# Kernel optimization log

Measured on AMD Instinct MI355X. Metric: run time of the kernel, lower is better.

Reference implementation:

```python
import jax, jax.numpy as jnp
import numpy as np

B, H, S, DK = 2, 16, 2048, 64
NEG = jnp.float32(-10000.0)


def setup_inputs() -> dict:
    key = jax.random.key(0)
    kq, kk, kv, km = jax.random.split(key, 4)
    query = jax.random.normal(kq, (B, H, S, DK), dtype=jnp.float32)
    k_ = jax.random.normal(kk, (B, H, S, DK), dtype=jnp.float32)
    value = jax.random.normal(kv, (B, H, S, DK), dtype=jnp.float32)
    mask = (jax.random.uniform(km, (B, 1, S, S)) > 0.5).astype(jnp.float32)
    return {"query": query, "key": k_, "value": value, "mask": mask, "d_k": DK}


def reference(query, key, value, mask, d_k):
    # scores: [B,H,S,S]
    scale = jnp.float32(1.0 / np.sqrt(d_k))
    scores = jnp.einsum('bhqd,bhkd->bhqk', query, key) * scale * mask
    # non-standard masking: keep only strictly positive masked scores
    scores = jnp.where(scores > 0, scores, NEG)
    attn = jax.nn.softmax(scores, axis=-1)
    return jnp.einsum('bhqk,bhkd->bhqd', attn, value)
```

## Files before the change

### kernel.cpp

```cpp
#include <hip/hip_runtime.h>
#include <hip/hip_bf16.h>
#include <math.h>

#define S_LEN 2048
#define D_KV  64
#define BQ    128
#define BK    64
#define LP    72
#define NW    8

typedef __attribute__((ext_vector_type(8))) short bh8;
typedef __attribute__((ext_vector_type(4))) short sh4;
typedef __attribute__((ext_vector_type(4))) float fx4;

__device__ __forceinline__ short f2bf(float f) {
    unsigned u = __builtin_bit_cast(unsigned, f);
    u += 0x7fffu + ((u >> 16) & 1u);
    return (short)(u >> 16);
}

__global__ __launch_bounds__(512, 4)
void attn_fwd(const float* __restrict__ Qg, const float* __restrict__ Kg,
              const float* __restrict__ Vg, const float* __restrict__ Mg,
              float* __restrict__ Og)
{
    __shared__ __align__(16) short k_lds[BK * LP];
    __shared__ __align__(16) short v_lds[D_KV * LP];
    __shared__ __align__(16) short p_lds[NW * 16 * LP];

    const int tid  = threadIdx.x;
    const int wave = tid >> 6;
    const int lane = tid & 63;
    const int g    = lane >> 4;
    const int c    = lane & 15;

    const int qt = blockIdx.x;
    const int bh = blockIdx.y;
    const int b  = bh >> 4;

    const int qw = qt * BQ + wave * 16;

    const float* Qp = Qg + ((size_t)bh * S_LEN + qw) * D_KV;
    const float* Kp = Kg + (size_t)bh * S_LEN * D_KV;
    const float* Vp = Vg + (size_t)bh * S_LEN * D_KV;
    const float* Mp = Mg + (size_t)b * S_LEN * S_LEN;
    float*       Op = Og + ((size_t)bh * S_LEN + qw) * D_KV;

    bh8 qf[2];
#pragma unroll
    for (int kc = 0; kc < 2; ++kc) {
        const float* src = Qp + c * D_KV + kc * 32 + g * 8;
        float4 a0 = *(const float4*)(src);
        float4 a1 = *(const float4*)(src + 4);
        bh8 f;
        f[0] = f2bf(a0.x * 0.125f); f[1] = f2bf(a0.y * 0.125f);
        f[2] = f2bf(a0.z * 0.125f); f[3] = f2bf(a0.w * 0.125f);
        f[4] = f2bf(a1.x * 0.125f); f[5] = f2bf(a1.y * 0.125f);
        f[6] = f2bf(a1.z * 0.125f); f[7] = f2bf(a1.w * 0.125f);
        qf[kc] = f;
    }

    fx4 o[4];
    float l_r[4];
#pragma unroll
    for (int u = 0; u < 4; ++u) { fx4 z = {0.f, 0.f, 0.f, 0.f}; o[u] = z; }
#pragma unroll
    for (int r = 0; r < 4; ++r) l_r[r] = 0.f;

    for (int kt = 0; kt < S_LEN; kt += BK) {
#pragma unroll
        for (int i = 0; i < 2; ++i) {
            int idx = tid + 512 * i;
            int kr  = idx >> 4;
            int db  = (idx & 15) * 4;
            float4 kv = *(const float4*)(Kp + (size_t)(kt + kr) * D_KV + db);
            sh4 s4;
            s4[0] = f2bf(kv.x); s4[1] = f2bf(kv.y);
            s4[2] = f2bf(kv.z); s4[3] = f2bf(kv.w);
            *(sh4*)&k_lds[kr * LP + db] = s4;
        }
        {
            int kr = lane;
#pragma unroll
            for (int i = 0; i < 2; ++i) {
                int db = wave * 8 + i * 4;
                float4 vv = *(const float4*)(Vp + (size_t)(kt + kr) * D_KV + db);
                v_lds[(db + 0) * LP + kr] = f2bf(vv.x);
                v_lds[(db + 1) * LP + kr] = f2bf(vv.y);
                v_lds[(db + 2) * LP + kr] = f2bf(vv.z);
                v_lds[(db + 3) * LP + kr] = f2bf(vv.w);
            }
        }
        __syncthreads();

        fx4 sacc[4];
#pragma unroll
        for (int t = 0; t < 4; ++t) { fx4 z = {0.f, 0.f, 0.f, 0.f}; sacc[t] = z; }
#pragma unroll
        for (int kc = 0; kc < 2; ++kc) {
#pragma unroll
            for (int t = 0; t < 4; ++t) {
                bh8 kf = *(const bh8*)&k_lds[(t * 16 + c) * LP + kc * 32 + g * 8];
                sacc[t] = __builtin_amdgcn_mfma_f32_16x16x32_bf16(qf[kc], kf, sacc[t], 0, 0, 0);
            }
        }

        const float* mbase = Mp + (size_t)(qw + g * 4) * S_LEN + kt + c;
        float mv[4][4];
#pragma unroll
        for (int t = 0; t < 4; ++t)
#pragma unroll
            for (int r = 0; r < 4; ++r)
                mv[t][r] = mbase[(size_t)r * S_LEN + t * 16];

        short* pw = &p_lds[wave * 16 * LP];
#pragma unroll
        for (int t = 0; t < 4; ++t)
#pragma unroll
            for (int r = 0; r < 4; ++r) {
                float tm = sacc[t][r] * mv[t][r];
                float p  = (tm > 0.f) ? __expf(tm) : 0.f;
                l_r[r] += p;
                pw[(g * 4 + r) * LP + t * 16 + c] = f2bf(p);
            }

#pragma unroll
        for (int kc = 0; kc < 2; ++kc) {
            bh8 pa = *(const bh8*)&pw[c * LP + kc * 32 + g * 8];
#pragma unroll
            for (int u = 0; u < 4; ++u) {
                bh8 vb = *(const bh8*)&v_lds[(u * 16 + c) * LP + kc * 32 + g * 8];
                o[u] = __builtin_amdgcn_mfma_f32_16x16x32_bf16(pa, vb, o[u], 0, 0, 0);
            }
        }
        __syncthreads();
    }

#pragma unroll
    for (int r = 0; r < 4; ++r) {
#pragma unroll
        for (int off = 8; off >= 1; off >>= 1)
            l_r[r] += __shfl_xor(l_r[r], off, 16);
    }

#pragma unroll
    for (int r = 0; r < 4; ++r) {
        float inv = 1.0f / l_r[r];
#pragma unroll
        for (int u = 0; u < 4; ++u)
            Op[(size_t)(g * 4 + r) * D_KV + u * 16 + c] = o[u][r] * inv;
    }
}

extern "C" void kernel_launch(void* const* d_in, const int* in_sizes, int n_in,
                              void* d_out, int out_size, void* d_ws, size_t ws_size,
                              hipStream_t stream) {
    const float* Q = (const float*)d_in[0];
    const float* K = (const float*)d_in[1];
    const float* V = (const float*)d_in[2];
    const float* M = (const float*)d_in[3];
    float*       O = (float*)d_out;
    dim3 grid(S_LEN / BQ, 32);
    attn_fwd<<<grid, 512, 0, stream>>>(Q, K, V, M, O);
}
```

Measured before the change: 188.6 us.

## Split KV range across wave groups, transpose MFMA, keep P in registers

Halves the query tile to 64 rows and splits the 2048-long key range between two groups of four waves, then merges partial outputs and row sums through shared memory at the end. Swaps the MFMA operand order so the probability tile comes out in the register layout needed as the B operand of the PV product, removing the P round-trip through LDS. It also moves K/V staging to XOR-swizzled LDS without padding, uses packed bf16 conversion instructions, and loads the mask as vector float4 rows. Costs include the extra merge step and more blocks contending for mask bandwidth.

```diff
diff --git a/kernel.cpp b/kernel.cpp
--- a/kernel.cpp
+++ b/kernel.cpp
@@ -1,154 +1,179 @@
 #include <hip/hip_runtime.h>
-#include <hip/hip_bf16.h>
 #include <math.h>
 
 #define S_LEN 2048
 #define D_KV  64
-#define BQ    128
+#define BQ    64
 #define BK    64
-#define LP    72
-#define NW    8
+#define KHALF 1024
 
 typedef __attribute__((ext_vector_type(8))) short bh8;
-typedef __attribute__((ext_vector_type(4))) short sh4;
 typedef __attribute__((ext_vector_type(4))) float fx4;
+typedef __attribute__((ext_vector_type(4))) unsigned int u32x4;
+typedef __attribute__((ext_vector_type(2))) unsigned int u32x2;
 
-__device__ __forceinline__ short f2bf(float f) {
-    unsigned u = __builtin_bit_cast(unsigned, f);
-    u += 0x7fffu + ((u >> 16) & 1u);
-    return (short)(u >> 16);
+__device__ __forceinline__ unsigned cvt2(float a, float b) {
+    unsigned r;
+    asm("v_cvt_pk_bf16_f32 %0, %1, %2" : "=v"(r) : "v"(a), "v"(b));
+    return r;
 }
 
-__global__ __launch_bounds__(512, 4)
+__device__ __forceinline__ int kswz(int row, int dkb) {
+    return ((row << 7) + dkb) ^ ((row & 7) << 4);
+}
+__device__ __forceinline__ int vswz(int d, int colb) {
+    return ((d << 7) + colb) ^ (((d >> 2) & 7) << 4);
+}
+
+__global__ __launch_bounds__(512, 6)
 void attn_fwd(const float* __restrict__ Qg, const float* __restrict__ Kg,
               const float* __restrict__ Vg, const float* __restrict__ Mg,
               float* __restrict__ Og)
 {
-    __shared__ __align__(16) short k_lds[BK * LP];
-    __shared__ __align__(16) short v_lds[D_KV * LP];
-    __shared__ __align__(16) short p_lds[NW * 16 * LP];
+    __shared__ __align__(16) char smem[32768];
 
     const int tid  = threadIdx.x;
     const int wave = tid >> 6;
     const int lane = tid & 63;
     const int g    = lane >> 4;
     const int c    = lane & 15;
+    const int kg   = wave >> 2;
+    const int tidg = tid & 255;
 
     const int qt = blockIdx.x;
     const int bh = blockIdx.y;
     const int b  = bh >> 4;
 
-    const int qw = qt * BQ + wave * 16;
+    const int qbase = qt * BQ + (wave & 3) * 16;
 
-    const float* Qp = Qg + ((size_t)bh * S_LEN + qw) * D_KV;
+    short* kb = (short*)(smem) + kg * 4096;
+    short* vb = (short*)(smem + 16384) + kg * 4096;
+
     const float* Kp = Kg + (size_t)bh * S_LEN * D_KV;
     const float* Vp = Vg + (size_t)bh * S_LEN * D_KV;
-    const float* Mp = Mg + (size_t)b * S_LEN * S_LEN;
-    float*       Op = Og + ((size_t)bh * S_LEN + qw) * D_KV;
+    const float* Qp = Qg + ((size_t)bh * S_LEN + qbase) * D_KV;
+    const float* mrow = Mg + (size_t)b * S_LEN * S_LEN
+                      + (size_t)(qbase + c) * S_LEN + g * 4;
 
     bh8 qf[2];
 #pragma unroll
     for (int kc = 0; kc < 2; ++kc) {
         const float* src = Qp + c * D_KV + kc * 32 + g * 8;
-        float4 a0 = *(const float4*)(src);
-        float4 a1 = *(const float4*)(src + 4);
-        bh8 f;
-        f[0] = f2bf(a0.x * 0.125f); f[1] = f2bf(a0.y * 0.125f);
-        f[2] = f2bf(a0.z * 0.125f); f[3] = f2bf(a0.w * 0.125f);
-        f[4] = f2bf(a1.x * 0.125f); f[5] = f2bf(a1.y * 0.125f);
-        f[6] = f2bf(a1.z * 0.125f); f[7] = f2bf(a1.w * 0.125f);
-        qf[kc] = f;
+        fx4 a0 = *(const fx4*)(src);
+        fx4 a1 = *(const fx4*)(src + 4);
+        u32x4 q4 = { cvt2(a0[0] * 0.125f, a0[1] * 0.125f),
+                     cvt2(a0[2] * 0.125f, a0[3] * 0.125f),
+                     cvt2(a1[0] * 0.125f, a1[1] * 0.125f),
+                     cvt2(a1[2] * 0.125f, a1[3] * 0.125f) };
+        qf[kc] = __builtin_bit_cast(bh8, q4);
     }
 
     fx4 o[4];
-    float l_r[4];
 #pragma unroll
     for (int u = 0; u < 4; ++u) { fx4 z = {0.f, 0.f, 0.f, 0.f}; o[u] = z; }
+    float l = 0.f;
+
+    const int vk0 = (tidg >> 4) << 2;
+    const int vd0 = (tidg & 15) << 2;
+    const int vcolb = (((vk0 & 15) >> 2) << 5) + ((vk0 >> 4) << 3);
+
+    for (int it = 0; it < 16; ++it) {
+        const int kt = kg * KHALF + it * BK;
+
 #pragma unroll
-    for (int r = 0; r < 4; ++r) l_r[r] = 0.f;
-
-    for (int kt = 0; kt < S_LEN; kt += BK) {
-#pragma unroll
-        for (int i = 0; i < 2; ++i) {
-            int idx = tid + 512 * i;
-            int kr  = idx >> 4;
-            int db  = (idx & 15) * 4;
-            float4 kv = *(const float4*)(Kp + (size_t)(kt + kr) * D_KV + db);
-            sh4 s4;
-            s4[0] = f2bf(kv.x); s4[1] = f2bf(kv.y);
-            s4[2] = f2bf(kv.z); s4[3] = f2bf(kv.w);
-            *(sh4*)&k_lds[kr * LP + db] = s4;
+        for (int i = 0; i < 4; ++i) {
+            const int idx = tidg + 256 * i;
+            const int kr  = idx >> 4;
+            const int de  = (idx & 15) << 2;
+            fx4 t4 = *(const fx4*)(Kp + (size_t)(kt + kr) * D_KV + de);
+            u32x2 w = { cvt2(t4[0], t4[1]), cvt2(t4[2], t4[3]) };
+            *(u32x2*)((char*)kb + kswz(kr, de << 1)) = w;
         }
         {
-            int kr = lane;
+            const float* vsrc = Vp + (size_t)(kt + vk0) * D_KV + vd0;
+            fx4 r0 = *(const fx4*)(vsrc);
+            fx4 r1 = *(const fx4*)(vsrc + D_KV);
+            fx4 r2 = *(const fx4*)(vsrc + 2 * D_KV);
+            fx4 r3 = *(const fx4*)(vsrc + 3 * D_KV);
 #pragma unroll
-            for (int i = 0; i < 2; ++i) {
-                int db = wave * 8 + i * 4;
-                float4 vv = *(const float4*)(Vp + (size_t)(kt + kr) * D_KV + db);
-                v_lds[(db + 0) * LP + kr] = f2bf(vv.x);
-                v_lds[(db + 1) * LP + kr] = f2bf(vv.y);
-                v_lds[(db + 2) * LP + kr] = f2bf(vv.z);
-                v_lds[(db + 3) * LP + kr] = f2bf(vv.w);
+            for (int i = 0; i < 4; ++i) {
+                u32x2 w = { cvt2(r0[i], r1[i]), cvt2(r2[i], r3[i]) };
+                *(u32x2*)((char*)vb + vswz(vd0 + i, vcolb)) = w;
             }
         }
         __syncthreads();
 
-        fx4 sacc[4];
+        fx4 mv[4];
 #pragma unroll
-        for (int t = 0; t < 4; ++t) { fx4 z = {0.f, 0.f, 0.f, 0.f}; sacc[t] = z; }
+        for (int t = 0; t < 4; ++t)
+            mv[t] = *(const fx4*)(mrow + kt + t * 16);
+
+        fx4 st[4];
+#pragma unroll
+        for (int t = 0; t < 4; ++t) { fx4 z = {0.f, 0.f, 0.f, 0.f}; st[t] = z; }
 #pragma unroll
         for (int kc = 0; kc < 2; ++kc) {
 #pragma unroll
             for (int t = 0; t < 4; ++t) {
-                bh8 kf = *(const bh8*)&k_lds[(t * 16 + c) * LP + kc * 32 + g * 8];
-                sacc[t] = __builtin_amdgcn_mfma_f32_16x16x32_bf16(qf[kc], kf, sacc[t], 0, 0, 0);
+                bh8 kf = *(const bh8*)((char*)kb + kswz(t * 16 + c, (kc << 6) + (g << 4)));
+                st[t] = __builtin_amdgcn_mfma_f32_16x16x32_bf16(kf, qf[kc], st[t], 0, 0, 0);
             }
         }
 
-        const float* mbase = Mp + (size_t)(qw + g * 4) * S_LEN + kt + c;
-        float mv[4][4];
+        unsigned pk[8];
 #pragma unroll
-        for (int t = 0; t < 4; ++t)
-#pragma unroll
-            for (int r = 0; r < 4; ++r)
-                mv[t][r] = mbase[(size_t)r * S_LEN + t * 16];
-
-        short* pw = &p_lds[wave * 16 * LP];
-#pragma unroll
-        for (int t = 0; t < 4; ++t)
-#pragma unroll
-            for (int r = 0; r < 4; ++r) {
-                float tm = sacc[t][r] * mv[t][r];
-                float p  = (tm > 0.f) ? __expf(tm) : 0.f;
-                l_r[r] += p;
-                pw[(g * 4 + r) * LP + t * 16 + c] = f2bf(p);
-            }
+        for (int t = 0; t < 4; ++t) {
+            float tm0 = st[t][0] * mv[t][0];
+            float tm1 = st[t][1] * mv[t][1];
+            float tm2 = st[t][2] * mv[t][2];
+            float tm3 = st[t][3] * mv[t][3];
+            float p0 = tm0 > 0.f ? __expf(tm0) : 0.f;
+            float p1 = tm1 > 0.f ? __expf(tm1) : 0.f;
+            float p2 = tm2 > 0.f ? __expf(tm2) : 0.f;
+            float p3 = tm3 > 0.f ? __expf(tm3) : 0.f;
+            l += (p0 + p1) + (p2 + p3);
+            pk[t * 2 + 0] = cvt2(p0, p1);
+            pk[t * 2 + 1] = cvt2(p2, p3);
+        }
 
 #pragma unroll
-        for (int kc = 0; kc < 2; ++kc) {
-            bh8 pa = *(const bh8*)&pw[c * LP + kc * 32 + g * 8];
+        for (int tp = 0; tp < 2; ++tp) {
+            u32x4 pq = { pk[tp * 4 + 0], pk[tp * 4 + 1],
+                         pk[tp * 4 + 2], pk[tp * 4 + 3] };
+            bh8 pp = __builtin_bit_cast(bh8, pq);
 #pragma unroll
             for (int u = 0; u < 4; ++u) {
-                bh8 vb = *(const bh8*)&v_lds[(u * 16 + c) * LP + kc * 32 + g * 8];
-                o[u] = __builtin_amdgcn_mfma_f32_16x16x32_bf16(pa, vb, o[u], 0, 0, 0);
+                bh8 vv = *(const bh8*)((char*)vb + vswz(u * 16 + c, (g << 5) + (tp << 4)));
+                o[u] = __builtin_amdgcn_mfma_f32_16x16x32_bf16(vv, pp, o[u], 0, 0, 0);
             }
         }
         __syncthreads();
     }
 
+    l += __shfl_xor(l, 16);
+    l += __shfl_xor(l, 32);
+
+    __syncthreads();
+    float* scr = (float*)smem;
+    if (wave >= 4) {
+        float* dst = scr + ((wave - 4) * 64 + lane) * 20;
 #pragma unroll
-    for (int r = 0; r < 4; ++r) {
+        for (int u = 0; u < 4; ++u) *(fx4*)(dst + u * 4) = o[u];
+        dst[16] = l;
+    }
+    __syncthreads();
+    if (wave < 4) {
+        const float* sp = scr + (wave * 64 + lane) * 20;
 #pragma unroll
-        for (int off = 8; off >= 1; off >>= 1)
-            l_r[r] += __shfl_xor(l_r[r], off, 16);
-    }
-
+        for (int u = 0; u < 4; ++u) o[u] += *(const fx4*)(sp + u * 4);
+        l += sp[16];
+        const float inv = 1.0f / l;
+        float* orow = Og + ((size_t)bh * S_LEN + qbase + c) * D_KV + g * 4;
 #pragma unroll
-    for (int r = 0; r < 4; ++r) {
-        float inv = 1.0f / l_r[r];
-#pragma unroll
-        for (int u = 0; u < 4; ++u)
-            Op[(size_t)(g * 4 + r) * D_KV + u * 16 + c] = o[u][r] * inv;
+        for (int u = 0; u < 4; ++u) {
+            fx4 r = o[u] * inv;
+            *(fx4*)(orow + u * 16) = r;
+        }
     }
 }
 
```

After: 288.8 us. +53.1%, slower.
